# Kernel tuning notes

Hardware: AMD Instinct MI355X
Metric: run time of the kernel (lower is better)

## Reference

```python
import jax, jax.numpy as jnp
import numpy as np

N_NODES, N_EDGES = 50000, 800000
D_NODE, D_EDGE, N_CLASSES, N_HEADS = 64, 64, 40, 4


def setup_inputs() -> dict:
    key = jax.random.key(0)
    ks = jax.random.split(key, 20)
    g = lambda k, shp: (jax.random.normal(k, shp, jnp.float32) * (1.0 / np.sqrt(shp[0])))
    inp = {
        "nodes": jax.random.normal(ks[0], (N_NODES, D_NODE), jnp.float32),
        "edges": jax.random.normal(ks[1], (N_EDGES, D_EDGE), jnp.float32),
        "edge_index": jax.random.randint(ks[2], (2, N_EDGES), 0, N_NODES, jnp.int32),
        # NodeAttention params
        "Wq_n": g(ks[3], (D_NODE, D_NODE)),
        "Wk_n": g(ks[4], (D_NODE, D_NODE)),
        "We_n": g(ks[5], (D_EDGE, D_NODE)),
        "Wv_n": g(ks[6], (D_NODE, D_NODE)),
        "Wo_n": g(ks[7], (D_NODE, D_NODE)),
        # EdgeAttention params
        "Wq_e": g(ks[8], (D_EDGE, D_EDGE)),
        "Wk_e": g(ks[9], (D_EDGE, D_EDGE)),
        "Wn_e": g(ks[10], (D_NODE, D_EDGE)),
        "Wv_e": g(ks[11], (D_EDGE, D_EDGE)),
        "Wo_e": g(ks[12], (D_EDGE, D_EDGE)),
        # classifier: Linear(2*d_node+d_edge -> d_edge), GELU, Linear(d_edge -> num_classes)
        "W1": g(ks[13], (2 * D_NODE + D_EDGE, D_EDGE)),
        "b1": jnp.zeros((D_EDGE,), jnp.float32),
        "W2": g(ks[14], (D_EDGE, N_CLASSES)),
        "b2": jnp.zeros((N_CLASSES,), jnp.float32),
    }
    return inp


def _segment_softmax(scores, seg, num_segments):
    # scores: [E, H], seg: [E] -> softmax over edges within each segment
    m = jax.ops.segment_max(scores, seg, num_segments)
    ex = jnp.exp(scores - m[seg])
    den = jax.ops.segment_sum(ex, seg, num_segments)
    return ex / (den[seg] + 1e-9)


def _forward(nodes, edges, edge_index, Wq_n, Wk_n, We_n, Wv_n, Wo_n,
             Wq_e, Wk_e, Wn_e, Wv_e, Wo_e, W1, b1, W2, b2):
    src, tgt = edge_index[0], edge_index[1]
    E = edges.shape[0]
    N = nodes.shape[0]
    Dh_n = D_NODE // N_HEADS
    Dh_e = D_EDGE // N_HEADS

    # ---- NodeAttention: nodes attend over incoming edges ----
    q = (nodes @ Wq_n).reshape(N, N_HEADS, Dh_n)
    k = ((nodes @ Wk_n)[src] + edges @ We_n).reshape(E, N_HEADS, Dh_n)
    v = (nodes @ Wv_n)[src].reshape(E, N_HEADS, Dh_n)
    s_n = (q[tgt] * k).sum(-1) / jnp.sqrt(jnp.float32(Dh_n))  # [E, H]
    a_n = _segment_softmax(s_n, tgt, N)
    msg = jax.ops.segment_sum(a_n[..., None] * v, tgt, N).reshape(N, D_NODE)
    new_nodes = nodes + msg @ Wo_n

    # ---- EdgeAttention: edges attend among edges sharing a source node ----
    qe = (edges @ Wq_e).reshape(E, N_HEADS, Dh_e)
    ke = (edges @ Wk_e + nodes[src] @ Wn_e).reshape(E, N_HEADS, Dh_e)
    ve = (edges @ Wv_e).reshape(E, N_HEADS, Dh_e)
    s_e = (qe * ke).sum(-1) / jnp.sqrt(jnp.float32(Dh_e))  # [E, H]
    a_e = _segment_softmax(s_e, src, N)
    pooled = jax.ops.segment_sum(a_e[..., None] * ve, src, N).reshape(N, D_EDGE)
    new_edges = edges + pooled[src] @ Wo_e

    # ---- edge-indexed gather + concat + 2-layer GELU MLP classifier ----
    combined = jnp.concatenate([new_nodes[src], new_nodes[tgt], new_edges], axis=-1)
    h = jax.nn.gelu(combined @ W1 + b1)
    return h @ W2 + b2  # [E, num_classes]


def reference(nodes, edges, edge_index, Wq_n, Wk_n, We_n, Wv_n, Wo_n,
              Wq_e, Wk_e, Wn_e, Wv_e, Wo_e, W1, b1, W2, b2):
    return _forward(nodes, edges, edge_index, Wq_n, Wk_n, We_n, Wv_n, Wo_n,
                    Wq_e, Wk_e, Wn_e, Wv_e, Wo_e, W1, b1, W2, b2)
```

## Files before the change

### kernel.cpp

```cpp
#include <hip/hip_runtime.h>
#include <cstdint>
#include <cstddef>

typedef unsigned short u16t;
typedef __attribute__((ext_vector_type(8))) short bf16x8;
typedef __attribute__((ext_vector_type(4))) float f32x4;

#define NNODES 50000
#define NEDGES 800000
#define NP 50176

#define MFMA(a, b, c) __builtin_amdgcn_mfma_f32_16x16x32_bf16((a), (b), (c), 0, 0, 0)

__device__ inline float b2f(short s) {
    union { float f; unsigned int u; } c;
    c.u = ((unsigned int)(unsigned short)s) << 16;
    return c.f;
}
__device__ inline short f2b(float f) {
    union { float f; unsigned int u; } c; c.f = f;
    unsigned int u = c.u;
    unsigned int r = (u + 0x7FFFu + ((u >> 16) & 1u)) >> 16;
    return (short)(unsigned short)r;
}
__device__ inline f32x4 zero4() { f32x4 z = {0.f, 0.f, 0.f, 0.f}; return z; }

__device__ inline bf16x8 ld8f(const float* p) {
    float4 a = *(const float4*)p;
    float4 b = *(const float4*)(p + 4);
    bf16x8 r;
    r[0] = f2b(a.x); r[1] = f2b(a.y); r[2] = f2b(a.z); r[3] = f2b(a.w);
    r[4] = f2b(b.x); r[5] = f2b(b.y); r[6] = f2b(b.z); r[7] = f2b(b.w);
    return r;
}

__device__ inline float gelu_f(float x) {
    float u = 0.7978845608028654f * (x + 0.044715f * x * x * x);
    float e = __expf(2.f * u);
    return 0.5f * x * (2.f - 2.f / (e + 1.f));
}

__global__ void k_init(float* __restrict__ msg, float* __restrict__ pooled,
                       float* __restrict__ d_n, float* __restrict__ d_e) {
    int i = blockIdx.x * 256 + threadIdx.x;
    if (i < NP * 64) { msg[i] = 0.f; pooled[i] = 0.f; }
    if (i < NP * 4)  { d_n[i] = 0.f; d_e[i] = 0.f; }
}

__global__ __launch_bounds__(256) void k_node_proj(
        const float* __restrict__ nodes,
        const float* __restrict__ Wq, const float* __restrict__ Wk,
        const float* __restrict__ Wv, const float* __restrict__ Wn,
        u16t* __restrict__ qn, u16t* __restrict__ kn,
        u16t* __restrict__ vn, u16t* __restrict__ nWn) {
    __shared__ __align__(16) u16t wt[256 * 72];
    {
        const float* Ws[4] = {Wq, Wk, Wv, Wn};
        for (int g = 0; g < 4; ++g) {
            const float* W = Ws[g];
            u16t* dst = wt + g * 64 * 72;
            for (int idx = threadIdx.x; idx < 4096; idx += 256) {
                int n = idx & 63, k = idx >> 6;
                dst[n * 72 + k] = (u16t)f2b(W[idx]);
            }
        }
    }
    __syncthreads();
    int l = threadIdx.x & 63, w = threadIdx.x >> 6;
    int q = l >> 4, c = l & 15;
    int r0 = blockIdx.x * 256 + w * 64;

    bf16x8 A[4][2];
#pragma unroll
    for (int st = 0; st < 4; ++st) {
        int row = r0 + st * 16 + c;
        if (row >= NNODES) row = NNODES - 1;
#pragma unroll
        for (int ks = 0; ks < 2; ++ks)
            A[st][ks] = ld8f(nodes + (size_t)row * 64 + ks * 32 + q * 8);
    }
    u16t* outs[4] = {qn, kn, vn, nWn};
    for (int cg = 0; cg < 4; ++cg) {
        bf16x8 B[2][4];
#pragma unroll
        for (int ks = 0; ks < 2; ++ks)
#pragma unroll
            for (int t = 0; t < 4; ++t)
                B[ks][t] = *(const bf16x8*)(wt + (cg * 64 + t * 16 + c) * 72 + ks * 32 + q * 8);
        float scale = (cg == 0) ? 0.25f : 1.0f;
        u16t* out = outs[cg];
#pragma unroll
        for (int st = 0; st < 4; ++st) {
            f32x4 acc[4];
#pragma unroll
            for (int t = 0; t < 4; ++t) acc[t] = zero4();
#pragma unroll
            for (int ks = 0; ks < 2; ++ks)
#pragma unroll
                for (int t = 0; t < 4; ++t)
                    acc[t] = MFMA(A[st][ks], B[ks][t], acc[t]);
#pragma unroll
            for (int r = 0; r < 4; ++r) {
                int row = r0 + st * 16 + q * 4 + r;
                if (row < NNODES) {
#pragma unroll
                    for (int t = 0; t < 4; ++t)
                        out[(size_t)row * 64 + t * 16 + c] = (u16t)f2b(acc[t][r] * scale);
                }
            }
        }
    }
}

__global__ __launch_bounds__(256) void k_edge_scores(
        const float* __restrict__ edges, const int* __restrict__ eidx,
        const float* __restrict__ WeN, const float* __restrict__ WqE, const float* __restrict__ WkE,
        const u16t* __restrict__ qn, const u16t* __restrict__ kn, const u16t* __restrict__ nWn,
        float* __restrict__ s_n, float* __restrict__ s_e,
        float* __restrict__ d_n, float* __restrict__ d_e) {
    __shared__ __align__(16) u16t wt[192 * 72];
    for (int idx = threadIdx.x; idx < 4096; idx += 256) {
        int n = idx & 63, k = idx >> 6;
        wt[n * 72 + k]         = (u16t)f2b(WeN[idx]);
        wt[(64 + n) * 72 + k]  = (u16t)f2b(0.25f * WqE[idx]);
        wt[(128 + n) * 72 + k] = (u16t)f2b(WkE[idx]);
    }
    __syncthreads();
    int l = threadIdx.x & 63, w = threadIdx.x >> 6;
    int q = l >> 4, c = l & 15;
    int rsel = c >> 2, tsel = c & 3;
    int e0 = blockIdx.x * 256 + w * 64;

    for (int st = 0; st < 4; ++st) {
        int eA = e0 + st * 16 + c;
        bf16x8 A0 = ld8f(edges + (size_t)eA * 64 + q * 8);
        bf16x8 A1 = ld8f(edges + (size_t)eA * 64 + 32 + q * 8);
        f32x4 aWe[4], aQe[4], aKe[4];
#pragma unroll
        for (int t = 0; t < 4; ++t) { aWe[t] = zero4(); aQe[t] = zero4(); aKe[t] = zero4(); }
#pragma unroll
        for (int t = 0; t < 4; ++t) {
            const u16t* b0 = wt + (t * 16 + c) * 72;
            const u16t* b1 = wt + (64 + t * 16 + c) * 72;
            const u16t* b2 = wt + (128 + t * 16 + c) * 72;
            aWe[t] = MFMA(A0, *(const bf16x8*)(b0 + q * 8), aWe[t]);
            aWe[t] = MFMA(A1, *(const bf16x8*)(b0 + 32 + q * 8), aWe[t]);
            aQe[t] = MFMA(A0, *(const bf16x8*)(b1 + q * 8), aQe[t]);
            aQe[t] = MFMA(A1, *(const bf16x8*)(b1 + 32 + q * 8), aQe[t]);
            aKe[t] = MFMA(A0, *(const bf16x8*)(b2 + q * 8), aKe[t]);
            aKe[t] = MFMA(A1, *(const bf16x8*)(b2 + 32 + q * 8), aKe[t]);
        }
        float kept_n = 0.f, kept_e = 0.f;
#pragma unroll
        for (int r = 0; r < 4; ++r) {
            int e = e0 + st * 16 + q * 4 + r;
            int sr = eidx[e], tg = eidx[NEDGES + e];
#pragma unroll
            for (int t = 0; t < 4; ++t) {
                int col = t * 16 + c;
                float pn = b2f((short)qn[(size_t)tg * 64 + col]) *
                           (b2f((short)kn[(size_t)sr * 64 + col]) + aWe[t][r]);
                float pe = aQe[t][r] * (aKe[t][r] + b2f((short)nWn[(size_t)sr * 64 + col]));
#pragma unroll
                for (int m = 1; m < 16; m <<= 1) {
                    pn += __shfl_xor(pn, m);
                    pe += __shfl_xor(pe, m);
                }
                if (r == rsel && t == tsel) { kept_n = pn; kept_e = pe; }
            }
        }
        int eL = e0 + st * 16 + (l >> 2);
        int srL = eidx[eL], tgL = eidx[NEDGES + eL];
        float exn = __expf(kept_n), exe = __expf(kept_e);
        size_t sbase = (size_t)(e0 + st * 16) * 4;
        s_n[sbase + l] = exn;
        s_e[sbase + l] = exe;
        unsafeAtomicAdd(&d_n[tgL * 4 + tsel], exn);
        unsafeAtomicAdd(&d_e[srL * 4 + tsel], exe);
    }
}

__global__ void k_invden(float* __restrict__ d_n, float* __restrict__ d_e) {
    int i = blockIdx.x * 256 + threadIdx.x;
    if (i < NNODES * 4) {
        d_n[i] = 1.f / (d_n[i] + 1e-9f);
        d_e[i] = 1.f / (d_e[i] + 1e-9f);
    }
}

__global__ __launch_bounds__(256) void k_node_scatter(
        const int* __restrict__ eidx, const float* __restrict__ s_n,
        const float* __restrict__ d_n, const u16t* __restrict__ vn,
        float* __restrict__ msg) {
    long long t = (long long)blockIdx.x * 256 + threadIdx.x;
    int e = (int)(t >> 6), j = (int)(t & 63);
    int sr = eidx[e], tg = eidx[NEDGES + e];
    int h = j >> 4;
    float a = s_n[(size_t)e * 4 + h] * d_n[tg * 4 + h];
    unsafeAtomicAdd(&msg[(size_t)tg * 64 + j], a * b2f((short)vn[(size_t)sr * 64 + j]));
}

__global__ __launch_bounds__(256) void k_edge_scatter(
        const float* __restrict__ edges, const int* __restrict__ eidx,
        const float* __restrict__ WvE,
        const float* __restrict__ s_e, const float* __restrict__ d_e,
        float* __restrict__ pooled) {
    __shared__ __align__(16) u16t wt[64 * 72];
    for (int idx = threadIdx.x; idx < 4096; idx += 256) {
        int n = idx & 63, k = idx >> 6;
        wt[n * 72 + k] = (u16t)f2b(WvE[idx]);
    }
    __syncthreads();
    int l = threadIdx.x & 63, w = threadIdx.x >> 6;
    int q = l >> 4, c = l & 15;
    int e0 = blockIdx.x * 256 + w * 64;
    for (int st = 0; st < 4; ++st) {
        int em = e0 + st * 16 + c;
        bf16x8 A0 = ld8f(edges + (size_t)em * 64 + q * 8);
        bf16x8 A1 = ld8f(edges + (size_t)em * 64 + 32 + q * 8);
        f32x4 acc[4];
#pragma unroll
        for (int t = 0; t < 4; ++t) acc[t] = zero4();
#pragma unroll
        for (int t = 0; t < 4; ++t) {
            const u16t* bp = wt + (t * 16 + c) * 72;
            acc[t] = MFMA(A0, *(const bf16x8*)(bp + q * 8), acc[t]);
            acc[t] = MFMA(A1, *(const bf16x8*)(bp + 32 + q * 8), acc[t]);
        }
#pragma unroll
        for (int r = 0; r < 4; ++r) {
            int e = e0 + st * 16 + q * 4 + r;
            int sr = eidx[e];
#pragma unroll
            for (int t = 0; t < 4; ++t) {
                float a = s_e[(size_t)e * 4 + t] * d_e[sr * 4 + t];
                unsafeAtomicAdd(&pooled[(size_t)sr * 64 + t * 16 + c], a * acc[t][r]);
            }
        }
    }
}

__global__ __launch_bounds__(256) void k_node_update(
        const float* __restrict__ Ain, const float* __restrict__ W,
        const float* __restrict__ base, u16t* __restrict__ out) {
    __shared__ __align__(16) u16t wt[64 * 72];
    for (int idx = threadIdx.x; idx < 4096; idx += 256) {
        int n = idx & 63, k = idx >> 6;
        wt[n * 72 + k] = (u16t)f2b(W[idx]);
    }
    __syncthreads();
    int l = threadIdx.x & 63, w = threadIdx.x >> 6;
    int q = l >> 4, c = l & 15;
    int r0 = blockIdx.x * 256 + w * 64;
    bf16x8 B[2][4];
#pragma unroll
    for (int ks = 0; ks < 2; ++ks)
#pragma unroll
        for (int t = 0; t < 4; ++t)
            B[ks][t] = *(const bf16x8*)(wt + (t * 16 + c) * 72 + ks * 32 + q * 8);
    for (int st = 0; st < 4; ++st) {
        int row = r0 + st * 16 + c;
        if (row >= NNODES) row = NNODES - 1;
        bf16x8 A[2];
#pragma unroll
        for (int ks = 0; ks < 2; ++ks)
            A[ks] = ld8f(Ain + (size_t)row * 64 + ks * 32 + q * 8);
        f32x4 acc[4];
#pragma unroll
        for (int t = 0; t < 4; ++t) acc[t] = zero4();
#pragma unroll
        for (int t = 0; t < 4; ++t) {
            acc[t] = MFMA(A[0], B[0][t], acc[t]);
            acc[t] = MFMA(A[1], B[1][t], acc[t]);
        }
#pragma unroll
        for (int r = 0; r < 4; ++r) {
            int rw = r0 + st * 16 + q * 4 + r;
            if (rw < NNODES) {
#pragma unroll
                for (int t = 0; t < 4; ++t) {
                    int col = t * 16 + c;
                    float v = acc[t][r];
                    if (base) v += base[(size_t)rw * 64 + col];
                    out[(size_t)rw * 64 + col] = (u16t)f2b(v);
                }
            }
        }
    }
}

__global__ __launch_bounds__(256) void k_classifier(
        const float* __restrict__ edges, const int* __restrict__ eidx,
        const u16t* __restrict__ newN, const u16t* __restrict__ pWo,
        const float* __restrict__ W1, const float* __restrict__ b1,
        const float* __restrict__ W2, const float* __restrict__ b2,
        float* __restrict__ out) {
    __shared__ __align__(16) u16t wt1[64 * 200];
    __shared__ __align__(16) u16t wt2[48 * 72];
    __shared__ __align__(16) u16t hbuf[4][16 * 72];
    for (int idx = threadIdx.x; idx < 192 * 64; idx += 256) {
        int n = idx & 63, k = idx >> 6;
        wt1[n * 200 + k] = (u16t)f2b(W1[idx]);
    }
    for (int idx = threadIdx.x; idx < 48 * 64; idx += 256) {
        int n = idx % 48, k = idx / 48;
        wt2[n * 72 + k] = (n < 40) ? (u16t)f2b(W2[k * 40 + n]) : (u16t)0;
    }
    __syncthreads();
    int l = threadIdx.x & 63, w = threadIdx.x >> 6;
    int q = l >> 4, c = l & 15;
    int e0 = blockIdx.x * 256 + w * 64;

    bf16x8 B1[6][4];
#pragma unroll
    for (int ks = 0; ks < 6; ++ks)
#pragma unroll
        for (int t = 0; t < 4; ++t)
            B1[ks][t] = *(const bf16x8*)(wt1 + (t * 16 + c) * 200 + ks * 32 + q * 8);
    bf16x8 B2[2][3];
#pragma unroll
    for (int ks = 0; ks < 2; ++ks)
#pragma unroll
        for (int t = 0; t < 3; ++t)
            B2[ks][t] = *(const bf16x8*)(wt2 + (t * 16 + c) * 72 + ks * 32 + q * 8);

    for (int st = 0; st < 4; ++st) {
        int em = e0 + st * 16 + c;
        int srm = eidx[em], tgm = eidx[NEDGES + em];
        bf16x8 A[6];
#pragma unroll
        for (int ks = 0; ks < 2; ++ks) {
            A[ks]     = *(const bf16x8*)(newN + (size_t)srm * 64 + ks * 32 + q * 8);
            A[2 + ks] = *(const bf16x8*)(newN + (size_t)tgm * 64 + ks * 32 + q * 8);
            const float* ep = edges + (size_t)em * 64 + ks * 32 + q * 8;
            float4 x0 = *(const float4*)ep;
            float4 x1 = *(const float4*)(ep + 4);
            bf16x8 y = *(const bf16x8*)(pWo + (size_t)srm * 64 + ks * 32 + q * 8);
            bf16x8 z;
            z[0] = f2b(x0.x + b2f(y[0])); z[1] = f2b(x0.y + b2f(y[1]));
            z[2] = f2b(x0.z + b2f(y[2])); z[3] = f2b(x0.w + b2f(y[3]));
            z[4] = f2b(x1.x + b2f(y[4])); z[5] = f2b(x1.y + b2f(y[5]));
            z[6] = f2b(x1.z + b2f(y[6])); z[7] = f2b(x1.w + b2f(y[7]));
            A[4 + ks] = z;
        }
        f32x4 acc1[4];
#pragma unroll
        for (int t = 0; t < 4; ++t) acc1[t] = zero4();
#pragma unroll
        for (int ks = 0; ks < 6; ++ks)
#pragma unroll
            for (int t = 0; t < 4; ++t)
                acc1[t] = MFMA(A[ks], B1[ks][t], acc1[t]);
#pragma unroll
        for (int t = 0; t < 4; ++t) {
            float bb = b1[t * 16 + c];
#pragma unroll
            for (int r = 0; r < 4; ++r) {
                float x = acc1[t][r] + bb;
                hbuf[w][(q * 4 + r) * 72 + t * 16 + c] = (u16t)f2b(gelu_f(x));
            }
        }
        bf16x8 A2[2];
#pragma unroll
        for (int ks = 0; ks < 2; ++ks)
            A2[ks] = *(const bf16x8*)(&hbuf[w][c * 72 + ks * 32 + q * 8]);
        f32x4 acc2[3];
#pragma unroll
        for (int t = 0; t < 3; ++t) acc2[t] = zero4();
#pragma unroll
        for (int ks = 0; ks < 2; ++ks)
#pragma unroll
            for (int t = 0; t < 3; ++t)
                acc2[t] = MFMA(A2[ks], B2[ks][t], acc2[t]);
#pragma unroll
        for (int r = 0; r < 4; ++r) {
            int e = e0 + st * 16 + q * 4 + r;
#pragma unroll
            for (int t = 0; t < 3; ++t) {
                int col = t * 16 + c;
                if (col < 40)
                    out[(size_t)e * 40 + col] = acc2[t][r] + b2[col];
            }
        }
    }
}

extern "C" void kernel_launch(void* const* d_in, const int* in_sizes, int n_in,
                              void* d_out, int out_size, void* d_ws, size_t ws_size,
                              hipStream_t stream) {
    if (n_in < 17) return;
    const float* nodes = (const float*)d_in[0];
    const float* edges = (const float*)d_in[1];
    const int*   eidx  = (const int*)d_in[2];
    const float* Wq_n = (const float*)d_in[3];
    const float* Wk_n = (const float*)d_in[4];
    const float* We_n = (const float*)d_in[5];
    const float* Wv_n = (const float*)d_in[6];
    const float* Wo_n = (const float*)d_in[7];
    const float* Wq_e = (const float*)d_in[8];
    const float* Wk_e = (const float*)d_in[9];
    const float* Wn_e = (const float*)d_in[10];
    const float* Wv_e = (const float*)d_in[11];
    const float* Wo_e = (const float*)d_in[12];
    const float* W1   = (const float*)d_in[13];
    const float* b1   = (const float*)d_in[14];
    const float* W2   = (const float*)d_in[15];
    const float* b2   = (const float*)d_in[16];
    float* out = (float*)d_out;

    float* ws = (float*)d_ws;
    size_t o = 0;
    u16t* qn  = (u16t*)(ws + o); o += (size_t)NP * 32;
    u16t* kn  = (u16t*)(ws + o); o += (size_t)NP * 32;
    u16t* vn  = (u16t*)(ws + o); o += (size_t)NP * 32;
    u16t* nWn = (u16t*)(ws + o); o += (size_t)NP * 32;
    float* d_n = ws + o; o += (size_t)NP * 4;
    float* d_e = ws + o; o += (size_t)NP * 4;
    float* msg    = ws + o; o += (size_t)NP * 64;
    float* pooled = ws + o; o += (size_t)NP * 64;
    float* s_n = ws + o; o += (size_t)NEDGES * 4;
    float* s_e = ws + o; o += (size_t)NEDGES * 4;
    u16t* newN = (u16t*)(ws + o); o += (size_t)NP * 32;
    u16t* pWo  = (u16t*)(ws + o); o += (size_t)NP * 32;
    if (ws_size < o * sizeof(float)) return;

    k_init<<<12544, 256, 0, stream>>>(msg, pooled, d_n, d_e);
    k_node_proj<<<196, 256, 0, stream>>>(nodes, Wq_n, Wk_n, Wv_n, Wn_e, qn, kn, vn, nWn);
    k_edge_scores<<<3125, 256, 0, stream>>>(edges, eidx, We_n, Wq_e, Wk_e,
                                            qn, kn, nWn, s_n, s_e, d_n, d_e);
    k_invden<<<782, 256, 0, stream>>>(d_n, d_e);
    k_node_scatter<<<200000, 256, 0, stream>>>(eidx, s_n, d_n, vn, msg);
    k_edge_scatter<<<3125, 256, 0, stream>>>(edges, eidx, Wv_e, s_e, d_e, pooled);
    k_node_update<<<196, 256, 0, stream>>>(msg, Wo_n, nodes, newN);
    k_node_update<<<196, 256, 0, stream>>>(pooled, Wo_e, nullptr, pWo);
    k_classifier<<<3125, 256, 0, stream>>>(edges, eidx, newN, pWo, W1, b1, W2, b2, out);
}
```

Before: 1.037 ms.

## Fuse edge scores and scatters, defer softmax normalization to node update

Merges the edge-score, inverse-denominator, node-scatter and edge-scatter kernels into one edge kernel. It accumulates unnormalized exp-weighted values into msg/pooled and divides by the per-node denominator when node_update reads its input. This removes the s_n/s_e round trips, a re-read of edges and several launches. It also replaces the per-element butterfly shuffle reductions with a 16-way transpose-reduce tree. Skipping the max subtraction was already true before; the deferred normalization is algebraically equivalent.

```diff
diff --git a/kernel.cpp b/kernel.cpp
--- a/kernel.cpp
+++ b/kernel.cpp
@@ -33,11 +33,34 @@
     r[4] = f2b(b.x); r[5] = f2b(b.y); r[6] = f2b(b.z); r[7] = f2b(b.w);
     return r;
 }
+__device__ inline bf16x8 ld8fs(const float* p, float s) {
+    float4 a = *(const float4*)p;
+    float4 b = *(const float4*)(p + 4);
+    bf16x8 r;
+    r[0] = f2b(a.x * s); r[1] = f2b(a.y * s); r[2] = f2b(a.z * s); r[3] = f2b(a.w * s);
+    r[4] = f2b(b.x * s); r[5] = f2b(b.y * s); r[6] = f2b(b.z * s); r[7] = f2b(b.w * s);
+    return r;
+}
 
 __device__ inline float gelu_f(float x) {
     float u = 0.7978845608028654f * (x + 0.044715f * x * x * x);
     float e = __expf(2.f * u);
     return 0.5f * x * (2.f - 2.f / (e + 1.f));
+}
+
+__device__ inline float tree16(float* a, int l) {
+#pragma unroll
+    for (int b = 0; b < 4; ++b) {
+        const int m = 1 << b;
+        const bool up = (l & m) != 0;
+#pragma unroll
+        for (int j = 0; j < (8 >> b); ++j) {
+            float keep = up ? a[2 * j + 1] : a[2 * j];
+            float send = up ? a[2 * j] : a[2 * j + 1];
+            a[j] = keep + __shfl_xor(send, m);
+        }
+    }
+    return a[0];
 }
 
 __global__ void k_init(float* __restrict__ msg, float* __restrict__ pooled,
@@ -112,137 +135,121 @@
     }
 }
 
-__global__ __launch_bounds__(256) void k_edge_scores(
+__global__ __launch_bounds__(256) void k_edge_fused(
         const float* __restrict__ edges, const int* __restrict__ eidx,
-        const float* __restrict__ WeN, const float* __restrict__ WqE, const float* __restrict__ WkE,
-        const u16t* __restrict__ qn, const u16t* __restrict__ kn, const u16t* __restrict__ nWn,
-        float* __restrict__ s_n, float* __restrict__ s_e,
-        float* __restrict__ d_n, float* __restrict__ d_e) {
-    __shared__ __align__(16) u16t wt[192 * 72];
+        const float* __restrict__ WeN, const float* __restrict__ WqE,
+        const float* __restrict__ WkE, const float* __restrict__ WvE,
+        const u16t* __restrict__ qn, const u16t* __restrict__ kn,
+        const u16t* __restrict__ nWn, const u16t* __restrict__ vn,
+        float* __restrict__ d_n, float* __restrict__ d_e,
+        float* __restrict__ msg, float* __restrict__ pooled) {
+    __shared__ __align__(16) u16t wt[256 * 72];
     for (int idx = threadIdx.x; idx < 4096; idx += 256) {
         int n = idx & 63, k = idx >> 6;
         wt[n * 72 + k]         = (u16t)f2b(WeN[idx]);
         wt[(64 + n) * 72 + k]  = (u16t)f2b(0.25f * WqE[idx]);
         wt[(128 + n) * 72 + k] = (u16t)f2b(WkE[idx]);
+        wt[(192 + n) * 72 + k] = (u16t)f2b(WvE[idx]);
     }
     __syncthreads();
     int l = threadIdx.x & 63, w = threadIdx.x >> 6;
     int q = l >> 4, c = l & 15;
-    int rsel = c >> 2, tsel = c & 3;
     int e0 = blockIdx.x * 256 + w * 64;
 
     for (int st = 0; st < 4; ++st) {
-        int eA = e0 + st * 16 + c;
+        int ebase = e0 + st * 16;
+        int eA = ebase + c;
         bf16x8 A0 = ld8f(edges + (size_t)eA * 64 + q * 8);
         bf16x8 A1 = ld8f(edges + (size_t)eA * 64 + 32 + q * 8);
-        f32x4 aWe[4], aQe[4], aKe[4];
-#pragma unroll
-        for (int t = 0; t < 4; ++t) { aWe[t] = zero4(); aQe[t] = zero4(); aKe[t] = zero4(); }
+
+        int sr_[4], tg_[4];
+#pragma unroll
+        for (int r = 0; r < 4; ++r) {
+            int e = ebase + q * 4 + r;
+            sr_[r] = eidx[e];
+            tg_[r] = eidx[NEDGES + e];
+        }
+        int eL = ebase + (l >> 2), hL = l & 3;
+        int srL = eidx[eL], tgL = eidx[NEDGES + eL];
+
+        f32x4 aQe[4], aKe[4];
+#pragma unroll
+        for (int t = 0; t < 4; ++t) { aQe[t] = zero4(); aKe[t] = zero4(); }
 #pragma unroll
         for (int t = 0; t < 4; ++t) {
-            const u16t* b0 = wt + (t * 16 + c) * 72;
             const u16t* b1 = wt + (64 + t * 16 + c) * 72;
             const u16t* b2 = wt + (128 + t * 16 + c) * 72;
-            aWe[t] = MFMA(A0, *(const bf16x8*)(b0 + q * 8), aWe[t]);
-            aWe[t] = MFMA(A1, *(const bf16x8*)(b0 + 32 + q * 8), aWe[t]);
             aQe[t] = MFMA(A0, *(const bf16x8*)(b1 + q * 8), aQe[t]);
             aQe[t] = MFMA(A1, *(const bf16x8*)(b1 + 32 + q * 8), aQe[t]);
             aKe[t] = MFMA(A0, *(const bf16x8*)(b2 + q * 8), aKe[t]);
             aKe[t] = MFMA(A1, *(const bf16x8*)(b2 + 32 + q * 8), aKe[t]);
         }
-        float kept_n = 0.f, kept_e = 0.f;
-#pragma unroll
-        for (int r = 0; r < 4; ++r) {
-            int e = e0 + st * 16 + q * 4 + r;
-            int sr = eidx[e], tg = eidx[NEDGES + e];
+        float pe[16];
+#pragma unroll
+        for (int r = 0; r < 4; ++r)
 #pragma unroll
             for (int t = 0; t < 4; ++t) {
                 int col = t * 16 + c;
-                float pn = b2f((short)qn[(size_t)tg * 64 + col]) *
-                           (b2f((short)kn[(size_t)sr * 64 + col]) + aWe[t][r]);
-                float pe = aQe[t][r] * (aKe[t][r] + b2f((short)nWn[(size_t)sr * 64 + col]));
-#pragma unroll
-                for (int m = 1; m < 16; m <<= 1) {
-                    pn += __shfl_xor(pn, m);
-                    pe += __shfl_xor(pe, m);
-                }
-                if (r == rsel && t == tsel) { kept_n = pn; kept_e = pe; }
-            }
-        }
-        int eL = e0 + st * 16 + (l >> 2);
-        int srL = eidx[eL], tgL = eidx[NEDGES + eL];
-        float exn = __expf(kept_n), exe = __expf(kept_e);
-        size_t sbase = (size_t)(e0 + st * 16) * 4;
-        s_n[sbase + l] = exn;
-        s_e[sbase + l] = exe;
-        unsafeAtomicAdd(&d_n[tgL * 4 + tsel], exn);
-        unsafeAtomicAdd(&d_e[srL * 4 + tsel], exe);
-    }
-}
-
-__global__ void k_invden(float* __restrict__ d_n, float* __restrict__ d_e) {
-    int i = blockIdx.x * 256 + threadIdx.x;
-    if (i < NNODES * 4) {
-        d_n[i] = 1.f / (d_n[i] + 1e-9f);
-        d_e[i] = 1.f / (d_e[i] + 1e-9f);
-    }
-}
-
-__global__ __launch_bounds__(256) void k_node_scatter(
-        const int* __restrict__ eidx, const float* __restrict__ s_n,
-        const float* __restrict__ d_n, const u16t* __restrict__ vn,
-        float* __restrict__ msg) {
-    long long t = (long long)blockIdx.x * 256 + threadIdx.x;
-    int e = (int)(t >> 6), j = (int)(t & 63);
-    int sr = eidx[e], tg = eidx[NEDGES + e];
-    int h = j >> 4;
-    float a = s_n[(size_t)e * 4 + h] * d_n[tg * 4 + h];
-    unsafeAtomicAdd(&msg[(size_t)tg * 64 + j], a * b2f((short)vn[(size_t)sr * 64 + j]));
-}
-
-__global__ __launch_bounds__(256) void k_edge_scatter(
-        const float* __restrict__ edges, const int* __restrict__ eidx,
-        const float* __restrict__ WvE,
-        const float* __restrict__ s_e, const float* __restrict__ d_e,
-        float* __restrict__ pooled) {
-    __shared__ __align__(16) u16t wt[64 * 72];
-    for (int idx = threadIdx.x; idx < 4096; idx += 256) {
-        int n = idx & 63, k = idx >> 6;
-        wt[n * 72 + k] = (u16t)f2b(WvE[idx]);
-    }
-    __syncthreads();
-    int l = threadIdx.x & 63, w = threadIdx.x >> 6;
-    int q = l >> 4, c = l & 15;
-    int e0 = blockIdx.x * 256 + w * 64;
-    for (int st = 0; st < 4; ++st) {
-        int em = e0 + st * 16 + c;
-        bf16x8 A0 = ld8f(edges + (size_t)em * 64 + q * 8);
-        bf16x8 A1 = ld8f(edges + (size_t)em * 64 + 32 + q * 8);
-        f32x4 acc[4];
-#pragma unroll
-        for (int t = 0; t < 4; ++t) acc[t] = zero4();
+                float ng = b2f((short)nWn[(size_t)sr_[r] * 64 + col]);
+                pe[r * 4 + t] = aQe[t][r] * (aKe[t][r] + ng);
+            }
+        float exe = __expf(tree16(pe, l));
+        unsafeAtomicAdd(&d_e[srL * 4 + hL], exe);
+
+        f32x4 aVe[4];
+#pragma unroll
+        for (int t = 0; t < 4; ++t) aVe[t] = zero4();
 #pragma unroll
         for (int t = 0; t < 4; ++t) {
-            const u16t* bp = wt + (t * 16 + c) * 72;
-            acc[t] = MFMA(A0, *(const bf16x8*)(bp + q * 8), acc[t]);
-            acc[t] = MFMA(A1, *(const bf16x8*)(bp + 32 + q * 8), acc[t]);
-        }
-#pragma unroll
-        for (int r = 0; r < 4; ++r) {
-            int e = e0 + st * 16 + q * 4 + r;
-            int sr = eidx[e];
+            const u16t* b3 = wt + (192 + t * 16 + c) * 72;
+            aVe[t] = MFMA(A0, *(const bf16x8*)(b3 + q * 8), aVe[t]);
+            aVe[t] = MFMA(A1, *(const bf16x8*)(b3 + 32 + q * 8), aVe[t]);
+        }
+#pragma unroll
+        for (int r = 0; r < 4; ++r)
 #pragma unroll
             for (int t = 0; t < 4; ++t) {
-                float a = s_e[(size_t)e * 4 + t] * d_e[sr * 4 + t];
-                unsafeAtomicAdd(&pooled[(size_t)sr * 64 + t * 16 + c], a * acc[t][r]);
-            }
+                float a = __shfl(exe, (l & 48) + r * 4 + t);
+                unsafeAtomicAdd(&pooled[(size_t)sr_[r] * 64 + t * 16 + c], a * aVe[t][r]);
+            }
+
+        f32x4 aWe[4];
+#pragma unroll
+        for (int t = 0; t < 4; ++t) aWe[t] = zero4();
+#pragma unroll
+        for (int t = 0; t < 4; ++t) {
+            const u16t* b0 = wt + (t * 16 + c) * 72;
+            aWe[t] = MFMA(A0, *(const bf16x8*)(b0 + q * 8), aWe[t]);
+            aWe[t] = MFMA(A1, *(const bf16x8*)(b0 + 32 + q * 8), aWe[t]);
+        }
+        float pn[16];
+#pragma unroll
+        for (int r = 0; r < 4; ++r)
+#pragma unroll
+            for (int t = 0; t < 4; ++t) {
+                int col = t * 16 + c;
+                float qg = b2f((short)qn[(size_t)tg_[r] * 64 + col]);
+                float kg = b2f((short)kn[(size_t)sr_[r] * 64 + col]);
+                pn[r * 4 + t] = qg * (kg + aWe[t][r]);
+            }
+        float exn = __expf(tree16(pn, l));
+        unsafeAtomicAdd(&d_n[tgL * 4 + hL], exn);
+
+#pragma unroll
+        for (int el = 0; el < 16; ++el) {
+            int sE = __shfl(srL, el << 2);
+            int tE = __shfl(tgL, el << 2);
+            float a = __shfl(exn, (el << 2) + (l >> 4));
+            float vv = b2f((short)vn[(size_t)sE * 64 + l]);
+            unsafeAtomicAdd(&msg[(size_t)tE * 64 + l], a * vv);
         }
     }
 }
 
 __global__ __launch_bounds__(256) void k_node_update(
-        const float* __restrict__ Ain, const float* __restrict__ W,
-        const float* __restrict__ base, u16t* __restrict__ out) {
+        const float* __restrict__ Ain, const float* __restrict__ den,
+        const float* __restrict__ W, const float* __restrict__ base,
+        u16t* __restrict__ out) {
     __shared__ __align__(16) u16t wt[64 * 72];
     for (int idx = threadIdx.x; idx < 4096; idx += 256) {
         int n = idx & 63, k = idx >> 6;
@@ -263,8 +270,10 @@
         if (row >= NNODES) row = NNODES - 1;
         bf16x8 A[2];
 #pragma unroll
-        for (int ks = 0; ks < 2; ++ks)
-            A[ks] = ld8f(Ain + (size_t)row * 64 + ks * 32 + q * 8);
+        for (int ks = 0; ks < 2; ++ks) {
+            float iv = 1.f / (den[row * 4 + ks * 2 + (q >> 1)] + 1e-9f);
+            A[ks] = ld8fs(Ain + (size_t)row * 64 + ks * 32 + q * 8, iv);
+        }
         f32x4 acc[4];
 #pragma unroll
         for (int t = 0; t < 4; ++t) acc[t] = zero4();
@@ -418,20 +427,15 @@
     float* d_e = ws + o; o += (size_t)NP * 4;
     float* msg    = ws + o; o += (size_t)NP * 64;
     float* pooled = ws + o; o += (size_t)NP * 64;
-    float* s_n = ws + o; o += (size_t)NEDGES * 4;
-    float* s_e = ws + o; o += (size_t)NEDGES * 4;
     u16t* newN = (u16t*)(ws + o); o += (size_t)NP * 32;
     u16t* pWo  = (u16t*)(ws + o); o += (size_t)NP * 32;
     if (ws_size < o * sizeof(float)) return;
 
     k_init<<<12544, 256, 0, stream>>>(msg, pooled, d_n, d_e);
     k_node_proj<<<196, 256, 0, stream>>>(nodes, Wq_n, Wk_n, Wv_n, Wn_e, qn, kn, vn, nWn);
-    k_edge_scores<<<3125, 256, 0, stream>>>(edges, eidx, We_n, Wq_e, Wk_e,
-                                            qn, kn, nWn, s_n, s_e, d_n, d_e);
-    k_invden<<<782, 256, 0, stream>>>(d_n, d_e);
-    k_node_scatter<<<200000, 256, 0, stream>>>(eidx, s_n, d_n, vn, msg);
-    k_edge_scatter<<<3125, 256, 0, stream>>>(edges, eidx, Wv_e, s_e, d_e, pooled);
-    k_node_update<<<196, 256, 0, stream>>>(msg, Wo_n, nodes, newN);
-    k_node_update<<<196, 256, 0, stream>>>(pooled, Wo_e, nullptr, pWo);
+    k_edge_fused<<<3125, 256, 0, stream>>>(edges, eidx, We_n, Wq_e, Wk_e, Wv_e,
+                                           qn, kn, nWn, vn, d_n, d_e, msg, pooled);
+    k_node_update<<<196, 256, 0, stream>>>(msg, d_n, Wo_n, nodes, newN);
+    k_node_update<<<196, 256, 0, stream>>>(pooled, d_e, Wo_e, nullptr, pWo);
     k_classifier<<<3125, 256, 0, stream>>>(edges, eidx, newN, pWo, W1, b1, W2, b2, out);
 }
```

After: 1.085 ms. +4.6%, slower.
